# Optimization experiments

Measured on AMD Instinct MI355X. Metric: run time of the kernel, lower is better.

The kernel has to match this reference:

```python
import jax, jax.numpy as jnp
import numpy as np

LEAKY = 0.2  # tf.nn.leaky_relu default alpha
E_SZ = [64, 64, 16]
F_SZ = [128, 128, 8]
N_MAPS, C, H, W = 64, 1, 32, 32
B = 8192


def _leaky(x):
    return jnp.where(x >= 0, x, LEAKY * x)


def func_theta(x, theta, sz, in_sz):
    # x: [B, in_sz]; theta: [B, total]; per-sample MLP with weights sliced from theta
    y = x
    offset = 0
    n = len(sz)
    for i, out_sz in enumerate(sz):
        w_sz = in_sz * out_sz
        Wm = theta[:, offset:offset + w_sz].reshape(-1, in_sz, out_sz)
        offset += w_sz
        b = theta[:, offset:offset + out_sz]
        offset += out_sz
        y = jnp.einsum('bi,bio->bo', y, Wm) + b
        if i < n - 1:
            y = _leaky(y)
        in_sz = out_sz
    return y


def setup_inputs() -> dict:
    key = jax.random.key(0)
    ks = jax.random.split(key, 16)

    def g(k, shape, scale):
        return (jax.random.normal(k, shape, dtype=jnp.float32) * scale)

    inp = {
        'indices': jax.random.randint(ks[0], (B,), 0, N_MAPS, dtype=jnp.int32),
        'states': jax.random.normal(ks[1], (B, 4), dtype=jnp.float32),
        'maps': jax.random.normal(ks[2], (N_MAPS, C, H, W), dtype=jnp.float32),
        'fc1_w': g(ks[3], (C * H * W, 256), 1.0 / np.sqrt(C * H * W)),
        'fc1_b': jnp.zeros((256,), jnp.float32),
        'fc2_w': g(ks[4], (256, 128), 1.0 / np.sqrt(256)),
        'fc2_b': jnp.zeros((128,), jnp.float32),
        'fc3_w': g(ks[5], (128, 128), 1.0 / np.sqrt(128)),
        'fc3_b': jnp.zeros((128,), jnp.float32),
        'bn_w': g(ks[6], (128, 32), 1.0 / np.sqrt(128)),
        'bn_b': jnp.zeros((32,), jnp.float32),
        'e_w': g(ks[7], (32, 5456), 1e-5),
        'e_b': g(ks[8], (5456,), 1e-3),
        'f_w': g(ks[9], (32, 21768), 1e-5),
        'f_b': g(ks[10], (21768,), 1e-3),
    }
    return inp


def reference(indices, states, maps, fc1_w, fc1_b, fc2_w, fc2_b, fc3_w, fc3_b,
              bn_w, bn_b, e_w, e_b, f_w, f_b):
    # gather maps per sample and flatten (NCHW -> NHWC transpose is a no-op after flatten
    # mathematically, but keep the exact data layout of the original)
    m = jnp.transpose(maps[indices], (0, 2, 3, 1)).astype(jnp.float32)  # [B,H,W,C]
    z = m.reshape(m.shape[0], -1)

    # hypernet trunk
    z = _leaky(z @ fc1_w + fc1_b)
    z = _leaky(z @ fc2_w + fc2_b)
    z = _leaky(z @ fc3_w + fc3_b)
    z = z @ bn_w + bn_b  # bottleneck, no activation
    theta_e = z @ e_w + e_b  # [B, 5456]
    theta_f = z @ f_w + f_b  # [B, 21768]

    S = states[:, 0:2]
    G = states[:, 2:4]
    e_s = func_theta(S, theta_e, E_SZ, 2)
    e_g = func_theta(G, theta_e, E_SZ, 2)
    zf = jnp.concatenate([e_s, e_g], axis=-1)  # [B, 32]
    ang = func_theta(zf, theta_f, F_SZ, 2 * E_SZ[-1])  # [B, 8]
    pts = jnp.concatenate([jnp.sin(ang), jnp.cos(ang)], axis=-1)  # [B, 16]
    return pts
```

## Files before the change

### kernel.cpp

```cpp
#include <hip/hip_runtime.h>
#include <hip/hip_bf16.h>


#define LEAKY 0.2f
#define NCLS 64
#define B_TOT 8192
#define NSLICE 8


__device__ __forceinline__ float lrelu(float x) { return x >= 0.f ? x : LEAKY * x; }

__global__ __launch_bounds__(256) void fc1_kernel(
    const float* __restrict__ maps,
    const float* __restrict__ fc1_w, const float* __restrict__ fc1_b,
    float* __restrict__ h1g)
{
    __shared__ __align__(16) float m[1024];
    __shared__ float red[256];
    const int c = blockIdx.x;
    const int s = blockIdx.y;
    const int t = threadIdx.x;

    ((float4*)m)[t] = ((const float4*)(maps + c * 1024))[t];
    __syncthreads();

    const int o  = t & 31;
    const int ks = t >> 5;
    const int og = s * 32 + o;
    const float* wp = fc1_w + og;
    float acc = 0.f;
#pragma unroll 16
    for (int i = 0; i < 128; ++i) {
        const int k = ks * 128 + i;
        acc += m[k] * wp[k * 256];
    }
    red[t] = acc;
    __syncthreads();
    if (t < 32) {
        float a = fc1_b[og];
#pragma unroll
        for (int r = 0; r < 8; ++r) a += red[r * 32 + t];
        h1g[c * 256 + og] = lrelu(a);
    }
}

__global__ __launch_bounds__(512) void mid_kernel(
    const float* __restrict__ h1g,
    const float* __restrict__ fc2_w, const float* __restrict__ fc2_b,
    const float* __restrict__ fc3_w, const float* __restrict__ fc3_b,
    const float* __restrict__ bn_w,  const float* __restrict__ bn_b,
    float* __restrict__ z)
{
    __shared__ float h1[256];
    __shared__ float red[512];
    __shared__ float h2[128];
    __shared__ float h3[128];
    const int c = blockIdx.x;
    const int t = threadIdx.x;
    if (t < 256) h1[t] = h1g[c * 256 + t];
    __syncthreads();
    {
        const int o = t & 127, ks = t >> 7;
        float acc = 0.f;
#pragma unroll 16
        for (int i = 0; i < 64; ++i) {
            const int k = ks * 64 + i;
            acc += h1[k] * fc2_w[k * 128 + o];
        }
        red[t] = acc;
    }
    __syncthreads();
    if (t < 128) h2[t] = lrelu(fc2_b[t] + red[t] + red[128 + t] + red[256 + t] + red[384 + t]);
    __syncthreads();
    {
        const int o = t & 127, ks = t >> 7;
        float acc = 0.f;
#pragma unroll
        for (int i = 0; i < 32; ++i) {
            const int k = ks * 32 + i;
            acc += h2[k] * fc3_w[k * 128 + o];
        }
        red[t] = acc;
    }
    __syncthreads();
    if (t < 128) h3[t] = lrelu(fc3_b[t] + red[t] + red[128 + t] + red[256 + t] + red[384 + t]);
    __syncthreads();
    {
        const int o = t & 31, ks = t >> 5;
        float acc = 0.f;
#pragma unroll
        for (int i = 0; i < 8; ++i) {
            const int k = ks * 8 + i;
            acc += h3[k] * bn_w[k * 32 + o];
        }
        red[t] = acc;
    }
    __syncthreads();
    if (t < 32) {
        float a = bn_b[t];
#pragma unroll
        for (int r = 0; r < 16; ++r) a += red[r * 32 + t];
        z[c * 32 + t] = a;
    }
}

__global__ __launch_bounds__(256) void theta_kernel(
    const float* __restrict__ z,
    const float* __restrict__ e_w, const float* __restrict__ e_b,
    const float* __restrict__ f_w, const float* __restrict__ f_b,
    float* __restrict__ th_e, float* __restrict__ th_f)
{
    __shared__ __align__(16) float zl[2048];
    const int t = threadIdx.x;
    ((float4*)zl)[t]       = ((const float4*)z)[t];
    ((float4*)zl)[t + 256] = ((const float4*)z)[t + 256];
    __syncthreads();

    int j = blockIdx.x * 256 + t;
    const int cbase = blockIdx.y * 16;
    const float* wbase;
    float* op;
    int stride;
    float bias;
    if (j < 5456) {
        wbase = e_w + j; bias = e_b[j]; op = th_e + j; stride = 5456;
    } else {
        const int jj = j - 5456;
        if (jj >= 21768) return;
        wbase = f_w + jj; bias = f_b[jj]; op = th_f + jj; stride = 21768;
    }
    float wk[32];
#pragma unroll
    for (int k = 0; k < 32; ++k) wk[k] = wbase[k * stride];

#pragma unroll
    for (int cc = 0; cc < 16; cc += 4) {
        const int c0 = cbase + cc;
        float a0 = bias, a1 = bias, a2 = bias, a3 = bias;
#pragma unroll
        for (int k4 = 0; k4 < 8; ++k4) {
            const float4 z0 = *(const float4*)&zl[(c0 + 0) * 32 + k4 * 4];
            const float4 z1 = *(const float4*)&zl[(c0 + 1) * 32 + k4 * 4];
            const float4 z2 = *(const float4*)&zl[(c0 + 2) * 32 + k4 * 4];
            const float4 z3 = *(const float4*)&zl[(c0 + 3) * 32 + k4 * 4];
            const float w0 = wk[k4 * 4], w1 = wk[k4 * 4 + 1];
            const float w2 = wk[k4 * 4 + 2], w3 = wk[k4 * 4 + 3];
            a0 += z0.x * w0 + z0.y * w1 + z0.z * w2 + z0.w * w3;
            a1 += z1.x * w0 + z1.y * w1 + z1.z * w2 + z1.w * w3;
            a2 += z2.x * w0 + z2.y * w1 + z2.z * w2 + z2.w * w3;
            a3 += z3.x * w0 + z3.y * w1 + z3.z * w2 + z3.w * w3;
        }
        op[(size_t)(c0 + 0) * stride] = a0;
        op[(size_t)(c0 + 1) * stride] = a1;
        op[(size_t)(c0 + 2) * stride] = a2;
        op[(size_t)(c0 + 3) * stride] = a3;
    }
}

__global__ __launch_bounds__(1024) void bucket_kernel(
    const int* __restrict__ idx, int* __restrict__ counts,
    int* __restrict__ offsets, int* __restrict__ perm)
{
    __shared__ int cnt[16][64];
    __shared__ int wcur[16][64];
    const int t = threadIdx.x;
    const int w = t >> 6;
    const int l = t & 63;
    cnt[w][l] = 0;
    __syncthreads();
    int my[8];
#pragma unroll
    for (int r = 0; r < 8; ++r) {
        my[r] = idx[r * 1024 + t];
        atomicAdd(&cnt[w][my[r]], 1);
    }
    __syncthreads();
    if (t < 64) {
        int run = 0;
#pragma unroll
        for (int w2 = 0; w2 < 16; ++w2) {
            const int v = cnt[w2][t];
            wcur[w2][t] = run;
            run += v;
        }
        counts[t] = run;
        int x = run;
        for (int d = 1; d < 64; d <<= 1) {
            const int y = __shfl_up(x, d, 64);
            if (t >= d) x += y;
        }
        const int basec = x - run;
        offsets[t] = basec;
#pragma unroll
        for (int w2 = 0; w2 < 16; ++w2) wcur[w2][t] += basec;
    }
    __syncthreads();
#pragma unroll
    for (int r = 0; r < 8; ++r) {
        const int p = atomicAdd(&wcur[w][my[r]], 1);
        perm[p] = r * 1024 + t;
    }
}

__global__ __launch_bounds__(256) void func_kernel(
    const float* __restrict__ states,
    const float* __restrict__ th_e_all, const float* __restrict__ th_f_all,
    const int* __restrict__ counts, const int* __restrict__ offsets,
    const int* __restrict__ perm, float* __restrict__ out)
{
    __shared__ __align__(16) float wbuf[8192];
    __shared__ __align__(16) float w3fb[1160];
    __shared__ __align__(16) float actA[2304];
    __shared__ __align__(16) float actB[2304];

    const int c = blockIdx.x;
    const int s = blockIdx.y;
    const int nb   = counts[c];
    const int base = offsets[c];
    const int chunk = (nb + NSLICE - 1) / NSLICE;
    const int k0 = s * chunk;
    const int k1 = (nb < k0 + chunk) ? nb : (k0 + chunk);
    const int cnt = (k1 > k0) ? (k1 - k0) : 0;
    if (cnt == 0) return;

    const float* te = th_e_all + (size_t)c * 5456;
    const float* tf = th_f_all + (size_t)c * 21768;

    const int t  = threadIdx.x;
    const int b  = t & 15;
    const int gf = t >> 4;
    const int vb = t & 31;
    const int ve = (t >> 4) & 1;
    const int ge = t >> 5;
    const int colf = gf * 8;
    const int cole = ge * 8;
    const int eoff = vb * 72;
    const int foff = b * 132;

    for (int j = t * 4; j < 1160; j += 1024)
        *(float4*)&w3fb[j] = *(const float4*)&tf[20608 + j];

    const int passes = (cnt + 15) >> 4;
    for (int p = 0; p < passes; ++p) {
        __syncthreads();

        for (int j = t * 4; j < 5392; j += 1024)
            *(float4*)&wbuf[j] = *(const float4*)&te[j];
        __syncthreads();

        const int kk = k0 + p * 16 + b;
        const bool valid = kk < k1;
        const int bi = valid ? perm[base + kk] : 0;
        const float2 sv = *(const float2*)&states[(size_t)bi * 4 + 2 * ve];

        {
            const float4 wa0 = *(const float4*)&wbuf[cole];
            const float4 wa1 = *(const float4*)&wbuf[cole + 4];
            const float4 wb0 = *(const float4*)&wbuf[64 + cole];
            const float4 wb1 = *(const float4*)&wbuf[64 + cole + 4];
            const float4 bb0 = *(const float4*)&wbuf[128 + cole];
            const float4 bb1 = *(const float4*)&wbuf[128 + cole + 4];
            float4 o0, o1;
            o0.x = lrelu(sv.x * wa0.x + sv.y * wb0.x + bb0.x);
            o0.y = lrelu(sv.x * wa0.y + sv.y * wb0.y + bb0.y);
            o0.z = lrelu(sv.x * wa0.z + sv.y * wb0.z + bb0.z);
            o0.w = lrelu(sv.x * wa0.w + sv.y * wb0.w + bb0.w);
            o1.x = lrelu(sv.x * wa1.x + sv.y * wb1.x + bb1.x);
            o1.y = lrelu(sv.x * wa1.y + sv.y * wb1.y + bb1.y);
            o1.z = lrelu(sv.x * wa1.z + sv.y * wb1.z + bb1.z);
            o1.w = lrelu(sv.x * wa1.w + sv.y * wb1.w + bb1.w);
            *(float4*)&actA[eoff + cole]     = o0;
            *(float4*)&actA[eoff + cole + 4] = o1;
        }
        __syncthreads();

        {
            float acc[8] = {0, 0, 0, 0, 0, 0, 0, 0};
#pragma unroll 4
            for (int i4 = 0; i4 < 16; ++i4) {
                const float4 y4 = *(const float4*)&actA[eoff + i4 * 4];
#pragma unroll
                for (int u = 0; u < 4; ++u) {
                    const int row = 192 + (i4 * 4 + u) * 64 + cole;
                    const float4 wA = *(const float4*)&wbuf[row];
                    const float4 wB = *(const float4*)&wbuf[row + 4];
                    const float yv = (&y4.x)[u];
                    acc[0] += yv * wA.x; acc[1] += yv * wA.y;
                    acc[2] += yv * wA.z; acc[3] += yv * wA.w;
                    acc[4] += yv * wB.x; acc[5] += yv * wB.y;
                    acc[6] += yv * wB.z; acc[7] += yv * wB.w;
                }
            }
            const float4 bA = *(const float4*)&wbuf[4288 + cole];
            const float4 bB = *(const float4*)&wbuf[4288 + cole + 4];
            float4 o0, o1;
            o0.x = lrelu(acc[0] + bA.x); o0.y = lrelu(acc[1] + bA.y);
            o0.z = lrelu(acc[2] + bA.z); o0.w = lrelu(acc[3] + bA.w);
            o1.x = lrelu(acc[4] + bB.x); o1.y = lrelu(acc[5] + bB.y);
            o1.z = lrelu(acc[6] + bB.z); o1.w = lrelu(acc[7] + bB.w);
            *(float4*)&actB[eoff + cole]     = o0;
            *(float4*)&actB[eoff + cole + 4] = o1;
        }
        __syncthreads();

        {
            const int col3 = ge * 2;
            float a0 = 0.f, a1 = 0.f;
#pragma unroll 4
            for (int i4 = 0; i4 < 16; ++i4) {
                const float4 y4 = *(const float4*)&actB[eoff + i4 * 4];
#pragma unroll
                for (int u = 0; u < 4; ++u) {
                    const int i = i4 * 4 + u;
                    const float yv = (&y4.x)[u];
                    a0 += yv * wbuf[4352 + i * 16 + col3];
                    a1 += yv * wbuf[4352 + i * 16 + col3 + 1];
                }
            }
            a0 += wbuf[5376 + col3];
            a1 += wbuf[5376 + col3 + 1];
            actA[foff + ve * 16 + col3]     = a0;
            actA[foff + ve * 16 + col3 + 1] = a1;
        }
        __syncthreads();

        for (int j = t * 4; j < 4224; j += 1024)
            *(float4*)&wbuf[j] = *(const float4*)&tf[j];
        __syncthreads();

        {
            float acc[8] = {0, 0, 0, 0, 0, 0, 0, 0};
#pragma unroll
            for (int i4 = 0; i4 < 8; ++i4) {
                const float4 y4 = *(const float4*)&actA[foff + i4 * 4];
#pragma unroll
                for (int u = 0; u < 4; ++u) {
                    const int row = (i4 * 4 + u) * 128 + colf;
                    const float4 wA = *(const float4*)&wbuf[row];
                    const float4 wB = *(const float4*)&wbuf[row + 4];
                    const float yv = (&y4.x)[u];
                    acc[0] += yv * wA.x; acc[1] += yv * wA.y;
                    acc[2] += yv * wA.z; acc[3] += yv * wA.w;
                    acc[4] += yv * wB.x; acc[5] += yv * wB.y;
                    acc[6] += yv * wB.z; acc[7] += yv * wB.w;
                }
            }
            const float4 bA = *(const float4*)&wbuf[4096 + colf];
            const float4 bB = *(const float4*)&wbuf[4096 + colf + 4];
            float4 o0, o1;
            o0.x = lrelu(acc[0] + bA.x); o0.y = lrelu(acc[1] + bA.y);
            o0.z = lrelu(acc[2] + bA.z); o0.w = lrelu(acc[3] + bA.w);
            o1.x = lrelu(acc[4] + bB.x); o1.y = lrelu(acc[5] + bB.y);
            o1.z = lrelu(acc[6] + bB.z); o1.w = lrelu(acc[7] + bB.w);
            *(float4*)&actB[foff + colf]     = o0;
            *(float4*)&actB[foff + colf + 4] = o1;
        }
        __syncthreads();

        {
            float acc[8] = {0, 0, 0, 0, 0, 0, 0, 0};
#pragma unroll
            for (int h = 0; h < 2; ++h) {
                if (h) __syncthreads();
                for (int j = t * 4; j < 8192; j += 1024)
                    *(float4*)&wbuf[j] = *(const float4*)&tf[4224 + h * 8192 + j];
                __syncthreads();
#pragma unroll 4
                for (int i4 = 0; i4 < 16; ++i4) {
                    const float4 y4 = *(const float4*)&actB[foff + h * 64 + i4 * 4];
#pragma unroll
                    for (int u = 0; u < 4; ++u) {
                        const int row = (i4 * 4 + u) * 128 + colf;
                        const float4 wA = *(const float4*)&wbuf[row];
                        const float4 wB = *(const float4*)&wbuf[row + 4];
                        const float yv = (&y4.x)[u];
                        acc[0] += yv * wA.x; acc[1] += yv * wA.y;
                        acc[2] += yv * wA.z; acc[3] += yv * wA.w;
                        acc[4] += yv * wB.x; acc[5] += yv * wB.y;
                        acc[6] += yv * wB.z; acc[7] += yv * wB.w;
                    }
                }
            }
            const float4 bA = *(const float4*)&w3fb[colf];
            const float4 bB = *(const float4*)&w3fb[colf + 4];
            float4 o0, o1;
            o0.x = lrelu(acc[0] + bA.x); o0.y = lrelu(acc[1] + bA.y);
            o0.z = lrelu(acc[2] + bA.z); o0.w = lrelu(acc[3] + bA.w);
            o1.x = lrelu(acc[4] + bB.x); o1.y = lrelu(acc[5] + bB.y);
            o1.z = lrelu(acc[6] + bB.z); o1.w = lrelu(acc[7] + bB.w);
            *(float4*)&actA[foff + colf]     = o0;
            *(float4*)&actA[foff + colf + 4] = o1;
        }
        __syncthreads();

        if (gf < 8) {
            float a = 0.f;
#pragma unroll 8
            for (int i4 = 0; i4 < 32; ++i4) {
                const float4 y4 = *(const float4*)&actA[foff + i4 * 4];
#pragma unroll
                for (int u = 0; u < 4; ++u)
                    a += (&y4.x)[u] * w3fb[128 + (i4 * 4 + u) * 8 + gf];
            }
            a += w3fb[1152 + gf];
            if (valid) {
                out[(size_t)bi * 16 + gf]     = __sinf(a);
                out[(size_t)bi * 16 + 8 + gf] = __cosf(a);
            }
        }
    }
}

extern "C" void kernel_launch(void* const* d_in, const int* in_sizes, int n_in,
                              void* d_out, int out_size, void* d_ws, size_t ws_size,
                              hipStream_t stream)
{
    const int*   indices = (const int*)  d_in[0];
    const float* states  = (const float*)d_in[1];
    const float* maps    = (const float*)d_in[2];
    const float* fc1_w   = (const float*)d_in[3];
    const float* fc1_b   = (const float*)d_in[4];
    const float* fc2_w   = (const float*)d_in[5];
    const float* fc2_b   = (const float*)d_in[6];
    const float* fc3_w   = (const float*)d_in[7];
    const float* fc3_b   = (const float*)d_in[8];
    const float* bn_w    = (const float*)d_in[9];
    const float* bn_b    = (const float*)d_in[10];
    const float* e_w     = (const float*)d_in[11];
    const float* e_b     = (const float*)d_in[12];
    const float* f_w     = (const float*)d_in[13];
    const float* f_b     = (const float*)d_in[14];
    float* out = (float*)d_out;

    float* ws   = (float*)d_ws;
    float* z    = ws;
    float* th_e = ws + 2048;
    float* th_f = ws + 351232;
    float* h1g  = ws + 1744384;
    int* counts  = (int*)(ws + 1760768);
    int* offsets = counts + 64;
    int* perm    = counts + 128;

    fc1_kernel<<<dim3(NCLS, 8), 256, 0, stream>>>(maps, fc1_w, fc1_b, h1g);
    mid_kernel<<<NCLS, 512, 0, stream>>>(h1g, fc2_w, fc2_b, fc3_w, fc3_b,
                                         bn_w, bn_b, z);
    bucket_kernel<<<1, 1024, 0, stream>>>(indices, counts, offsets, perm);
    theta_kernel<<<dim3((5456 + 21768 + 255) / 256, 4), 256, 0, stream>>>(
        z, e_w, e_b, f_w, f_b, th_e, th_f);
    func_kernel<<<dim3(NCLS, NSLICE), 256, 0, stream>>>(
        states, th_e, th_f, counts, offsets, perm, out);
}
```

Before: 145.5 us.

## Fuse backbone MLP and bucketing into one kernel, widen func kernel blocks

Merges fc1, the mid MLP layers and the index bucketing into a single 65-block launch, with one extra block doing the bucketing. This removes two launches and the h1 round trip through global memory. The theta grid is doubled along the class axis, so each block handles 8 classes instead of 16. The func kernel moves to 512 threads covering 32 samples per pass with fewer slices, loads the e-weights once before the loop, and streams the f-weights in smaller chunks. In exchange, fc1 now runs on only 64 blocks for the whole layer, and the larger shared activation buffers may lower occupancy.

```diff
diff --git a/kernel.cpp b/kernel.cpp
--- a/kernel.cpp
+++ b/kernel.cpp
@@ -5,92 +5,131 @@
 #define LEAKY 0.2f
 #define NCLS 64
 #define B_TOT 8192
-#define NSLICE 8
+#define NSLICE 4
 
 
 __device__ __forceinline__ float lrelu(float x) { return x >= 0.f ? x : LEAKY * x; }
 
-__global__ __launch_bounds__(256) void fc1_kernel(
+__global__ __launch_bounds__(1024) void backbone_bucket_kernel(
     const float* __restrict__ maps,
     const float* __restrict__ fc1_w, const float* __restrict__ fc1_b,
-    float* __restrict__ h1g)
-{
-    __shared__ __align__(16) float m[1024];
-    __shared__ float red[256];
-    const int c = blockIdx.x;
-    const int s = blockIdx.y;
-    const int t = threadIdx.x;
-
-    ((float4*)m)[t] = ((const float4*)(maps + c * 1024))[t];
-    __syncthreads();
-
-    const int o  = t & 31;
-    const int ks = t >> 5;
-    const int og = s * 32 + o;
-    const float* wp = fc1_w + og;
-    float acc = 0.f;
-#pragma unroll 16
-    for (int i = 0; i < 128; ++i) {
-        const int k = ks * 128 + i;
-        acc += m[k] * wp[k * 256];
-    }
-    red[t] = acc;
-    __syncthreads();
-    if (t < 32) {
-        float a = fc1_b[og];
-#pragma unroll
-        for (int r = 0; r < 8; ++r) a += red[r * 32 + t];
-        h1g[c * 256 + og] = lrelu(a);
-    }
-}
-
-__global__ __launch_bounds__(512) void mid_kernel(
-    const float* __restrict__ h1g,
     const float* __restrict__ fc2_w, const float* __restrict__ fc2_b,
     const float* __restrict__ fc3_w, const float* __restrict__ fc3_b,
     const float* __restrict__ bn_w,  const float* __restrict__ bn_b,
-    float* __restrict__ z)
+    float* __restrict__ z,
+    const int* __restrict__ idx, int* __restrict__ counts,
+    int* __restrict__ offsets, int* __restrict__ perm)
 {
+    __shared__ float m[1024];
+    __shared__ float red[1024];
     __shared__ float h1[256];
-    __shared__ float red[512];
     __shared__ float h2[128];
     __shared__ float h3[128];
+    __shared__ int cnt[16][64];
+    __shared__ int wcur[16][64];
+
+    const int t = threadIdx.x;
+
+    if (blockIdx.x == 64) {
+        const int w = t >> 6;
+        cnt[w][t & 63] = 0;
+        __syncthreads();
+        int my[8];
+#pragma unroll
+        for (int r = 0; r < 8; ++r) {
+            my[r] = idx[r * 1024 + t];
+            atomicAdd(&cnt[w][my[r]], 1);
+        }
+        __syncthreads();
+        if (t < 64) {
+            int run = 0;
+#pragma unroll
+            for (int w2 = 0; w2 < 16; ++w2) {
+                const int v = cnt[w2][t];
+                wcur[w2][t] = run;
+                run += v;
+            }
+            counts[t] = run;
+            int x = run;
+            for (int d = 1; d < 64; d <<= 1) {
+                const int y = __shfl_up(x, d, 64);
+                if (t >= d) x += y;
+            }
+            const int basec = x - run;
+            offsets[t] = basec;
+#pragma unroll
+            for (int w2 = 0; w2 < 16; ++w2) wcur[w2][t] += basec;
+        }
+        __syncthreads();
+#pragma unroll
+        for (int r = 0; r < 8; ++r) {
+            const int p = atomicAdd(&wcur[w][my[r]], 1);
+            perm[p] = r * 1024 + t;
+        }
+        return;
+    }
+
     const int c = blockIdx.x;
-    const int t = threadIdx.x;
-    if (t < 256) h1[t] = h1g[c * 256 + t];
+    m[t] = maps[(size_t)c * 1024 + t];
+    __syncthreads();
+
+    {
+        const int o = t & 255, ks = t >> 8;
+        const float* wp = fc1_w + o;
+        float acc = 0.f;
+#pragma unroll 8
+        for (int i = 0; i < 256; ++i) {
+            const int k = ks * 256 + i;
+            acc += m[k] * wp[(size_t)k * 256];
+        }
+        red[t] = acc;
+    }
+    __syncthreads();
+    if (t < 256)
+        h1[t] = lrelu(fc1_b[t] + red[t] + red[256 + t] + red[512 + t] + red[768 + t]);
     __syncthreads();
     {
         const int o = t & 127, ks = t >> 7;
         float acc = 0.f;
-#pragma unroll 16
-        for (int i = 0; i < 64; ++i) {
-            const int k = ks * 64 + i;
+#pragma unroll
+        for (int i = 0; i < 32; ++i) {
+            const int k = ks * 32 + i;
             acc += h1[k] * fc2_w[k * 128 + o];
         }
         red[t] = acc;
     }
     __syncthreads();
-    if (t < 128) h2[t] = lrelu(fc2_b[t] + red[t] + red[128 + t] + red[256 + t] + red[384 + t]);
+    if (t < 128) {
+        float a = fc2_b[t];
+#pragma unroll
+        for (int r = 0; r < 8; ++r) a += red[r * 128 + t];
+        h2[t] = lrelu(a);
+    }
     __syncthreads();
     {
         const int o = t & 127, ks = t >> 7;
         float acc = 0.f;
 #pragma unroll
-        for (int i = 0; i < 32; ++i) {
-            const int k = ks * 32 + i;
+        for (int i = 0; i < 16; ++i) {
+            const int k = ks * 16 + i;
             acc += h2[k] * fc3_w[k * 128 + o];
         }
         red[t] = acc;
     }
     __syncthreads();
-    if (t < 128) h3[t] = lrelu(fc3_b[t] + red[t] + red[128 + t] + red[256 + t] + red[384 + t]);
+    if (t < 128) {
+        float a = fc3_b[t];
+#pragma unroll
+        for (int r = 0; r < 8; ++r) a += red[r * 128 + t];
+        h3[t] = lrelu(a);
+    }
     __syncthreads();
     {
         const int o = t & 31, ks = t >> 5;
         float acc = 0.f;
 #pragma unroll
-        for (int i = 0; i < 8; ++i) {
-            const int k = ks * 8 + i;
+        for (int i = 0; i < 4; ++i) {
+            const int k = ks * 4 + i;
             acc += h3[k] * bn_w[k * 32 + o];
         }
         red[t] = acc;
@@ -99,7 +138,7 @@
     if (t < 32) {
         float a = bn_b[t];
 #pragma unroll
-        for (int r = 0; r < 16; ++r) a += red[r * 32 + t];
+        for (int r = 0; r < 32; ++r) a += red[r * 32 + t];
         z[c * 32 + t] = a;
     }
 }
@@ -117,7 +156,7 @@
     __syncthreads();
 
     int j = blockIdx.x * 256 + t;
-    const int cbase = blockIdx.y * 16;
+    const int cbase = blockIdx.y * 8;
     const float* wbase;
     float* op;
     int stride;
@@ -131,10 +170,10 @@
     }
     float wk[32];
 #pragma unroll
-    for (int k = 0; k < 32; ++k) wk[k] = wbase[k * stride];
-
-#pragma unroll
-    for (int cc = 0; cc < 16; cc += 4) {
+    for (int k = 0; k < 32; ++k) wk[k] = wbase[(size_t)k * stride];
+
+#pragma unroll
+    for (int cc = 0; cc < 8; cc += 4) {
         const int c0 = cbase + cc;
         float a0 = bias, a1 = bias, a2 = bias, a3 = bias;
 #pragma unroll
@@ -157,61 +196,19 @@
     }
 }
 
-__global__ __launch_bounds__(1024) void bucket_kernel(
-    const int* __restrict__ idx, int* __restrict__ counts,
-    int* __restrict__ offsets, int* __restrict__ perm)
-{
-    __shared__ int cnt[16][64];
-    __shared__ int wcur[16][64];
-    const int t = threadIdx.x;
-    const int w = t >> 6;
-    const int l = t & 63;
-    cnt[w][l] = 0;
-    __syncthreads();
-    int my[8];
-#pragma unroll
-    for (int r = 0; r < 8; ++r) {
-        my[r] = idx[r * 1024 + t];
-        atomicAdd(&cnt[w][my[r]], 1);
-    }
-    __syncthreads();
-    if (t < 64) {
-        int run = 0;
-#pragma unroll
-        for (int w2 = 0; w2 < 16; ++w2) {
-            const int v = cnt[w2][t];
-            wcur[w2][t] = run;
-            run += v;
-        }
-        counts[t] = run;
-        int x = run;
-        for (int d = 1; d < 64; d <<= 1) {
-            const int y = __shfl_up(x, d, 64);
-            if (t >= d) x += y;
-        }
-        const int basec = x - run;
-        offsets[t] = basec;
-#pragma unroll
-        for (int w2 = 0; w2 < 16; ++w2) wcur[w2][t] += basec;
-    }
-    __syncthreads();
-#pragma unroll
-    for (int r = 0; r < 8; ++r) {
-        const int p = atomicAdd(&wcur[w][my[r]], 1);
-        perm[p] = r * 1024 + t;
-    }
-}
-
-__global__ __launch_bounds__(256) void func_kernel(
+#define ESTRIDE 68
+#define FSTRIDE 132
+
+__global__ __launch_bounds__(512) void func_kernel(
     const float* __restrict__ states,
     const float* __restrict__ th_e_all, const float* __restrict__ th_f_all,
     const int* __restrict__ counts, const int* __restrict__ offsets,
     const int* __restrict__ perm, float* __restrict__ out)
 {
-    __shared__ __align__(16) float wbuf[8192];
+    __shared__ __align__(16) float wbuf[5392];
     __shared__ __align__(16) float w3fb[1160];
-    __shared__ __align__(16) float actA[2304];
-    __shared__ __align__(16) float actB[2304];
+    __shared__ __align__(16) float actA[4352];
+    __shared__ __align__(16) float actB[4352];
 
     const int c = blockIdx.x;
     const int s = blockIdx.y;
@@ -227,28 +224,31 @@
     const float* tf = th_f_all + (size_t)c * 21768;
 
     const int t  = threadIdx.x;
-    const int b  = t & 15;
-    const int gf = t >> 4;
-    const int vb = t & 31;
-    const int ve = (t >> 4) & 1;
-    const int ge = t >> 5;
+    const int b  = t & 31;
+    const int ve = (t >> 5) & 1;
+    const int vb = t & 63;
+    const int ge = t >> 6;
+    const int gf = t >> 5;
+    const int cole = ge * 8;
     const int colf = gf * 8;
-    const int cole = ge * 8;
-    const int eoff = vb * 72;
-    const int foff = b * 132;
-
-    for (int j = t * 4; j < 1160; j += 1024)
+    const int eoff = vb * ESTRIDE;
+    const int foff = b * FSTRIDE;
+
+    for (int j = t * 4; j < 1160; j += 2048)
         *(float4*)&w3fb[j] = *(const float4*)&tf[20608 + j];
-
-    const int passes = (cnt + 15) >> 4;
+    for (int j = t * 4; j < 5392; j += 2048)
+        *(float4*)&wbuf[j] = *(const float4*)&te[j];
+
+    const int passes = (cnt + 31) >> 5;
     for (int p = 0; p < passes; ++p) {
         __syncthreads();
-
-        for (int j = t * 4; j < 5392; j += 1024)
-            *(float4*)&wbuf[j] = *(const float4*)&te[j];
-        __syncthreads();
-
-        const int kk = k0 + p * 16 + b;
+        if (p) {
+            for (int j = t * 4; j < 5392; j += 2048)
+                *(float4*)&wbuf[j] = *(const float4*)&te[j];
+            __syncthreads();
+        }
+
+        const int kk = k0 + p * 32 + b;
         const bool valid = kk < k1;
         const int bi = valid ? perm[base + kk] : 0;
         const float2 sv = *(const float2*)&states[(size_t)bi * 4 + 2 * ve];
@@ -324,7 +324,7 @@
         }
         __syncthreads();
 
-        for (int j = t * 4; j < 4224; j += 1024)
+        for (int j = t * 4; j < 4224; j += 2048)
             *(float4*)&wbuf[j] = *(const float4*)&tf[j];
         __syncthreads();
 
@@ -360,14 +360,14 @@
         {
             float acc[8] = {0, 0, 0, 0, 0, 0, 0, 0};
 #pragma unroll
-            for (int h = 0; h < 2; ++h) {
+            for (int h = 0; h < 4; ++h) {
                 if (h) __syncthreads();
-                for (int j = t * 4; j < 8192; j += 1024)
-                    *(float4*)&wbuf[j] = *(const float4*)&tf[4224 + h * 8192 + j];
+                for (int j = t * 4; j < 4096; j += 2048)
+                    *(float4*)&wbuf[j] = *(const float4*)&tf[4224 + h * 4096 + j];
                 __syncthreads();
 #pragma unroll 4
-                for (int i4 = 0; i4 < 16; ++i4) {
-                    const float4 y4 = *(const float4*)&actB[foff + h * 64 + i4 * 4];
+                for (int i4 = 0; i4 < 8; ++i4) {
+                    const float4 y4 = *(const float4*)&actB[foff + h * 32 + i4 * 4];
 #pragma unroll
                     for (int u = 0; u < 4; ++u) {
                         const int row = (i4 * 4 + u) * 128 + colf;
@@ -436,17 +436,15 @@
     float* z    = ws;
     float* th_e = ws + 2048;
     float* th_f = ws + 351232;
-    float* h1g  = ws + 1744384;
-    int* counts  = (int*)(ws + 1760768);
+    int* counts  = (int*)(ws + 1744384);
     int* offsets = counts + 64;
     int* perm    = counts + 128;
 
-    fc1_kernel<<<dim3(NCLS, 8), 256, 0, stream>>>(maps, fc1_w, fc1_b, h1g);
-    mid_kernel<<<NCLS, 512, 0, stream>>>(h1g, fc2_w, fc2_b, fc3_w, fc3_b,
-                                         bn_w, bn_b, z);
-    bucket_kernel<<<1, 1024, 0, stream>>>(indices, counts, offsets, perm);
-    theta_kernel<<<dim3((5456 + 21768 + 255) / 256, 4), 256, 0, stream>>>(
+    backbone_bucket_kernel<<<65, 1024, 0, stream>>>(
+        maps, fc1_w, fc1_b, fc2_w, fc2_b, fc3_w, fc3_b, bn_w, bn_b, z,
+        indices, counts, offsets, perm);
+    theta_kernel<<<dim3(107, 8), 256, 0, stream>>>(
         z, e_w, e_b, f_w, f_b, th_e, th_f);
-    func_kernel<<<dim3(NCLS, NSLICE), 256, 0, stream>>>(
+    func_kernel<<<dim3(NCLS, NSLICE), 512, 0, stream>>>(
         states, th_e, th_f, counts, offsets, perm, out);
 }
```

Result: faster. 141.6 us (-2.7%).
